# Optimization experiments

Hardware: AMD Instinct MI355X
Metric: run time of the kernel (lower is better)

The kernel has to match this reference:

```python
import jax, jax.numpy as jnp
import numpy as np

N = 4096   # num_nodes == nb_items
E = 3      # num_edge types
C = 2      # num_channels
D = 128    # basket_embed_dim
RU = 128   # rnn_units
B = 32     # batch size
L = 20     # max_seq_length
ALPHA = 0.5


def _gtconv(W, A):
    # softmax over edge types, then channel-weighted combine of adjacencies
    f = jax.nn.softmax(W, axis=1)              # [C, E]
    return jnp.einsum('ce,enm->cnm', f, A)     # [C, N, N]


def _normalize(H):
    # remove self loops, then column-degree (in-degree) inverse normalization
    eye = jnp.eye(H.shape[-1], dtype=H.dtype)
    Hn = H * (1.0 - eye)
    deg = Hn.sum(axis=1)                        # scatter_add over col -> [C, N]
    dinv = jnp.where(deg == 0, jnp.zeros_like(deg), 1.0 / deg)
    dinv = jax.lax.stop_gradient(dinv)          # original computes deg under no_grad
    return Hn * dinv[:, None, :]


def _lstm(x, h0, c0, W_ih, W_hh, b_ih, b_hh):
    # single-layer batch-first LSTM, torch gate order (i, f, g, o)
    def step(carry, xt):
        h, c = carry
        z = xt @ W_ih.T + b_ih + h @ W_hh.T + b_hh
        i, f, g, o = jnp.split(z, 4, axis=-1)
        c = jax.nn.sigmoid(f) * c + jax.nn.sigmoid(i) * jnp.tanh(g)
        h = jax.nn.sigmoid(o) * jnp.tanh(c)
        return (h, c), h
    _, ys = jax.lax.scan(step, (h0, c0), jnp.swapaxes(x, 0, 1))
    return jnp.swapaxes(ys, 0, 1)               # [B, L, RU]


def setup_inputs():
    key = jax.random.key(0)
    k = jax.random.split(key, 12)
    A = jax.random.uniform(k[0], (E, N, N), jnp.float32) * (2.0 / N)
    seqs = (jax.random.uniform(k[1], (B, L, N)) < 0.02).astype(jnp.float32)
    seq_len = jax.random.randint(k[2], (B,), 1, L + 1)
    h0 = jnp.zeros((B, RU), jnp.float32)
    c0 = jnp.zeros((B, RU), jnp.float32)
    W1a = 1.0 + 0.1 * jax.random.normal(k[3], (C, E), jnp.float32)
    W1b = 1.0 + 0.1 * jax.random.normal(k[4], (C, E), jnp.float32)
    W2 = 1.0 + 0.1 * jax.random.normal(k[5], (C, E), jnp.float32)
    I_B = jnp.ones((N,), jnp.float32) / N
    lin_w = jax.random.normal(k[6], (C, D, N), jnp.float32) / np.sqrt(N).astype(np.float32)
    lin_b = jnp.zeros((C, D), jnp.float32)
    proj_w = jax.random.normal(k[7], (D, C * D), jnp.float32) / np.sqrt(C * D).astype(np.float32)
    proj_b = jnp.zeros((D,), jnp.float32)
    W_ih = jax.random.normal(k[8], (4 * RU, D), jnp.float32) / np.sqrt(D).astype(np.float32)
    W_hh = jax.random.normal(k[9], (4 * RU, RU), jnp.float32) / np.sqrt(RU).astype(np.float32)
    b_ih = jnp.zeros((4 * RU,), jnp.float32)
    b_hh = jnp.zeros((4 * RU,), jnp.float32)
    h2item_w = jax.random.normal(k[10], (N, RU), jnp.float32) / np.sqrt(RU).astype(np.float32)
    return dict(A=A, seqs=seqs, seq_len=seq_len, h0=h0, c0=c0, W1a=W1a, W1b=W1b,
                W2=W2, I_B=I_B, lin_w=lin_w, lin_b=lin_b, proj_w=proj_w, proj_b=proj_b,
                W_ih=W_ih, W_hh=W_hh, b_ih=b_ih, b_hh=b_hh, h2item_w=h2item_w)


def reference(A, seqs, seq_len, h0, c0, W1a, W1b, W2, I_B, lin_w, lin_b,
              proj_w, proj_b, W_ih, W_hh, b_ih, b_hh, h2item_w):
    # layer 0 (first=True): H[c] = conv1(A)[c] @ conv2(A)[c]  (spspmm, dense form)
    H = jnp.einsum('cij,cjk->cik', _gtconv(W1a, A), _gtconv(W1b, A))
    # layer 1: H[c] = norm(H)[c] @ conv(A)[c]
    H = jnp.einsum('cij,cjk->cik', _normalize(H), _gtconv(W2, A))

    x = seqs.reshape(-1, N)                     # [B*L, nb_items]
    v = jax.nn.relu(I_B)                        # diag(I_B) after relu
    enc = []
    for i in range(C):
        xh = jax.nn.relu(x @ H[i])
        if i == 0:
            e = jax.nn.relu(x * v) + xh         # note: channel-0 formula differs
        else:
            e = jax.nn.relu(x * v + xh)
        enc.append(e @ lin_w[i].T + lin_b[i])
    enc = jnp.concatenate(enc, axis=1)          # [B*L, C*D]
    baskets = (enc @ proj_w.T + proj_b).reshape(B, L, D)

    lstm_out = _lstm(baskets, h0, c0, W_ih, W_hh, b_ih, b_hh)
    idx = jnp.arange(B) * L + (seq_len - 1)
    last = lstm_out.reshape(-1, RU)[idx]        # [B, RU]
    probs = jax.nn.sigmoid(last @ h2item_w.T)   # [B, nb_items]
    return (1.0 - ALPHA) * probs + ALPHA * (probs * v)
```

## Files before the change

### kernel.cpp

```cpp
#include <hip/hip_runtime.h>


typedef float  f4v  __attribute__((ext_vector_type(4)));
typedef short  s8v  __attribute__((ext_vector_type(8)));
typedef unsigned short u16;
typedef unsigned int u32;
typedef u32    u2v  __attribute__((ext_vector_type(2)));
typedef u32    u4v  __attribute__((ext_vector_type(4)));

#define NN 4096
#define MM 640

__device__ __forceinline__ u16 f2bf(float f){
  unsigned int u = __float_as_uint(f);
  u += 0x7FFFu + ((u>>16)&1u);
  return (u16)(u>>16);
}
__device__ __forceinline__ float bf2f(u16 h){ return __uint_as_float(((unsigned int)h)<<16); }
__device__ __forceinline__ float sigm(float x){ return 1.f/(1.f+__expf(-x)); }

__device__ __forceinline__ u32 pkbf(float lo, float hi){
  u32 r;
  asm("v_cvt_pk_bf16_f32 %0, %1, %2" : "=v"(r) : "v"(lo), "v"(hi));
  return r;
}

__device__ __forceinline__ void gload16(const void* g, void* l){
  __builtin_amdgcn_global_load_lds((const __attribute__((address_space(1))) unsigned int*)g,
                                   (__attribute__((address_space(3))) unsigned int*)l, 16, 0, 0);
}

__device__ __forceinline__ void softmax23(const float* __restrict__ W, float f[2][3]){
  #pragma unroll
  for (int c=0;c<2;c++){
    float a=W[c*3+0], b=W[c*3+1], d=W[c*3+2];
    float m=fmaxf(a,fmaxf(b,d));
    float ea=__expf(a-m), eb=__expf(b-m), ed=__expf(d-m);
    float s=1.f/(ea+eb+ed);
    f[c][0]=ea*s; f[c][1]=eb*s; f[c][2]=ed*s;
  }
}

__global__ __launch_bounds__(256)
void k_combine_all(const float* __restrict__ A, const float* __restrict__ W1a,
                   const float* __restrict__ W1b, const float* __restrict__ W2,
                   u16* __restrict__ C1, u16* __restrict__ C2t,
                   u16* __restrict__ C3t, float* __restrict__ r)
{
  __shared__ u16 t2[64][72];
  __shared__ u16 t3[64][72];
  __shared__ float rs[2][64];
  const int tid = threadIdx.x, lane = tid&63;
  const int n0 = blockIdx.x*64, m0 = blockIdx.y*64;
  float fa[2][3], fb[2][3], fc[2][3];
  softmax23(W1a, fa); softmax23(W1b, fb); softmax23(W2, fc);
  if (tid < 128) rs[tid>>6][tid&63] = 0.f;
  const int mb = tid>>4, nb = tid&15;
  f4v a0[4], a1[4], a2[4];
  #pragma unroll
  for (int j=0;j<4;j++){
    const float* ap = A + (size_t)(m0+mb*4+j)*NN + n0 + nb*4;
    a0[j] = *(const f4v*)ap;
    a1[j] = *(const f4v*)(ap + (size_t)NN*NN);
    a2[j] = *(const f4v*)(ap + 2*(size_t)NN*NN);
  }
  #pragma unroll
  for (int c=0;c<2;c++){
    float rp[4] = {};
    #pragma unroll
    for (int j=0;j<4;j++){
      f4v v1 = fa[c][0]*a0[j] + fa[c][1]*a1[j] + fa[c][2]*a2[j];
      u2v o = { pkbf(v1[0],v1[1]), pkbf(v1[2],v1[3]) };
      *(u2v*)(C1 + ((size_t)c*NN + m0+mb*4+j)*NN + n0 + nb*4) = o;
      #pragma unroll
      for (int k=0;k<4;k++) rp[k] += v1[k];
    }
    #pragma unroll
    for (int jj=0;jj<4;jj++){
      f4v c2v, c3v;
      #pragma unroll
      for (int j=0;j<4;j++){
        c2v[j] = fb[c][0]*a0[j][jj] + fb[c][1]*a1[j][jj] + fb[c][2]*a2[j][jj];
        c3v[j] = fc[c][0]*a0[j][jj] + fc[c][1]*a1[j][jj] + fc[c][2]*a2[j][jj];
      }
      *(u2v*)&t2[nb*4+jj][mb*4] = (u2v){ pkbf(c2v[0],c2v[1]), pkbf(c2v[2],c2v[3]) };
      *(u2v*)&t3[nb*4+jj][mb*4] = (u2v){ pkbf(c3v[0],c3v[1]), pkbf(c3v[2],c3v[3]) };
    }
    __syncthreads();
    #pragma unroll
    for (int rep=0;rep<2;rep++){
      const int rw = rep*32 + (tid>>3), l8 = tid&7;
      *(u4v*)(C2t + ((size_t)c*NN + n0+rw)*NN + m0 + l8*8) = *(const u4v*)&t2[rw][l8*8];
      *(u4v*)(C3t + ((size_t)c*NN + n0+rw)*NN + m0 + l8*8) = *(const u4v*)&t3[rw][l8*8];
    }
    #pragma unroll
    for (int k=0;k<4;k++){
      float v = rp[k];
      v += __shfl_xor(v,16); v += __shfl_xor(v,32);
      if (lane < 16) atomicAdd(&rs[c][nb*4+k], v);
    }
    __syncthreads();
  }
  if (tid < 128) atomicAdd(&r[(size_t)(tid>>6)*NN + n0 + (tid&63)], rs[tid>>6][tid&63]);
}

__global__ __launch_bounds__(256)
void k_sparse_y(const float* __restrict__ seqs, const u16* __restrict__ C1,
                u16* __restrict__ y)
{
  __shared__ int idxl[512];
  __shared__ int scan[256];
  const int tid = threadIdx.x, row = blockIdx.x;
  const float* xr = seqs + (size_t)row*NN;
  int runbase = 0;
  #pragma unroll
  for (int it=0; it<4; ++it){
    f4v v = *(const f4v*)(xr + it*1024 + tid*4);
    int flg[4], loc = 0;
    #pragma unroll
    for (int k=0;k<4;k++){ flg[k] = (v[k] > 0.5f); loc += flg[k]; }
    scan[tid] = loc;
    __syncthreads();
    #pragma unroll
    for (int off=1; off<256; off<<=1){
      int t = (tid>=off) ? scan[tid-off] : 0;
      __syncthreads();
      scan[tid] += t;
      __syncthreads();
    }
    int pos = runbase + scan[tid] - loc;
    #pragma unroll
    for (int k=0;k<4;k++)
      if (flg[k]){ if (pos < 512) idxl[pos] = it*1024 + tid*4 + k; pos++; }
    runbase += scan[255];
    __syncthreads();
  }
  const int nz = runbase < 512 ? runbase : 512;
  float acc0[16], acc1[16];
  #pragma unroll
  for (int k=0;k<16;k++){ acc0[k]=0.f; acc1[k]=0.f; }
  const int cb = tid*16;
  s8v ca, cb8, cc8, cd8;
  if (nz > 0){
    const u16* r0 = C1 + (size_t)idxl[0]*NN + cb;
    const u16* r1 = r0 + (size_t)NN*NN;
    ca=*(const s8v*)r0; cb8=*(const s8v*)(r0+8); cc8=*(const s8v*)r1; cd8=*(const s8v*)(r1+8);
  }
  for (int p=0;p<nz;++p){
    const int pn = (p+1<nz)? p+1 : p;
    const u16* r0 = C1 + (size_t)idxl[pn]*NN + cb;
    const u16* r1 = r0 + (size_t)NN*NN;
    s8v na=*(const s8v*)r0, nb=*(const s8v*)(r0+8), nc=*(const s8v*)r1, nd=*(const s8v*)(r1+8);
    #pragma unroll
    for (int k=0;k<8;k++){
      acc0[k]   += bf2f((u16)ca[k]);
      acc0[8+k] += bf2f((u16)cb8[k]);
      acc1[k]   += bf2f((u16)cc8[k]);
      acc1[8+k] += bf2f((u16)cd8[k]);
    }
    ca=na; cb8=nb; cc8=nc; cd8=nd;
  }
  u4v o0, o1;
  #pragma unroll
  for (int k=0;k<4;k++){
    o0[k] = pkbf(acc0[2*k], acc0[2*k+1]);
    o1[k] = pkbf(acc0[8+2*k], acc0[9+2*k]);
  }
  u16* y0 = y + (size_t)row*NN + cb;
  *(u4v*)y0 = o0; *(u4v*)(y0+8) = o1;
  #pragma unroll
  for (int k=0;k<4;k++){
    o0[k] = pkbf(acc1[2*k], acc1[2*k+1]);
    o1[k] = pkbf(acc1[8+2*k], acc1[9+2*k]);
  }
  u16* y1 = y0 + (size_t)MM*NN;
  *(u4v*)y1 = o0; *(u4v*)(y1+8) = o1;
}

__global__ __launch_bounds__(256)
void k_diagdeg(const u16* __restrict__ C1, const u16* __restrict__ C2t,
               const float* __restrict__ r, float* __restrict__ diag1,
               float* __restrict__ dinv)
{
  const int tid = threadIdx.x, lane = tid&63;
  const int gw = blockIdx.x*4 + (tid>>6);
  const int c = gw>>12, k = gw&4095;
  const u16* p1 = C1  + ((size_t)c*NN + k)*NN;
  const u16* p2 = C2t + ((size_t)c*NN + k)*NN;
  const float* pr = r + (size_t)c*NN;
  float dd = 0.f, dg = 0.f;
  for (int it=0; it<8; ++it){
    const int j = it*512 + lane*8;
    s8v v1 = *(const s8v*)(p1+j);
    s8v v2 = *(const s8v*)(p2+j);
    f4v r0 = *(const f4v*)(pr+j);
    f4v r1 = *(const f4v*)(pr+j+4);
    #pragma unroll
    for (int q=0;q<8;q++){
      float c2 = bf2f((u16)v2[q]);
      dd += bf2f((u16)v1[q]) * c2;
      dg += ((q<4)? r0[q] : r1[q-4]) * c2;
    }
  }
  #pragma unroll
  for (int m=1;m<64;m<<=1){ dd += __shfl_xor(dd, m); dg += __shfl_xor(dg, m); }
  if (lane==0){
    float deg = dg - dd;
    diag1[(size_t)c*NN+k] = dd;
    dinv[(size_t)c*NN+k]  = (deg==0.f) ? 0.f : 1.f/deg;
  }
}

__global__ __launch_bounds__(256)
void k_gemm_sk(const u16* __restrict__ Xb, const u16* __restrict__ Bt,
               float* __restrict__ part)
{
  __shared__ u16 As[2][128*32];
  __shared__ u16 Bs[2][128*32];
  const int tid = threadIdx.x, lane = tid&63, w = tid>>6;
  const int g = blockIdx.x;
  const int xcd = g & 7, q = g >> 3;
  const int m = q % 5, p = q / 5;
  const int nh = p & 3, ks = (p>>2)&3, c = (p>>4)&1;
  const int m0 = m*128, n0 = (nh*8 + xcd)*128, kb = ks*1024;
  const u16* Ab = Xb + (size_t)c*MM*NN;
  const u16* Bb = Bt + (size_t)c*NN*NN;
  const int srow = lane>>2;
  const int scol = ((lane&3) ^ (srow&3))*8;
  const int fr = lane&15, c0 = lane>>4;
  const int wm = (w>>1)*64, wn = (w&1)*64;
  f4v acc[4][4] = {};
  auto STAGE = [&](int buf, int k0){
    #pragma unroll
    for (int i=0;i<2;i++){
      const int rb = i*64 + w*16;
      gload16(Ab + (size_t)(m0 + rb + srow)*NN + k0 + scol, (void*)&As[buf][rb*32]);
      gload16(Bb + (size_t)(n0 + rb + srow)*NN + k0 + scol, (void*)&Bs[buf][rb*32]);
    }
  };
  STAGE(0, kb);
  __syncthreads();
  int cur = 0;
  for (int k0=0;k0<1024;k0+=32){
    if (k0+32 < 1024) STAGE(cur^1, kb+k0+32);
    s8v a[4], b[4];
    #pragma unroll
    for (int t=0;t<4;t++){
      const int ra = wm + t*16 + fr;
      a[t] = *(const s8v*)&As[cur][ra*32 + ((c0 ^ (ra&3))*8)];
      const int rb2 = wn + t*16 + fr;
      b[t] = *(const s8v*)&Bs[cur][rb2*32 + ((c0 ^ (rb2&3))*8)];
    }
    #pragma unroll
    for (int i=0;i<4;i++)
      #pragma unroll
      for (int j=0;j<4;j++)
        acc[i][j] = __builtin_amdgcn_mfma_f32_16x16x32_bf16(a[i], b[j], acc[i][j], 0, 0, 0);
    __syncthreads();
    cur ^= 1;
  }
  float* pb = part + (size_t)(c*4+ks)*MM*NN;
  #pragma unroll
  for (int i=0;i<4;i++){
    #pragma unroll
    for (int j=0;j<4;j++){
      const int col = n0 + wn + j*16 + fr;
      #pragma unroll
      for (int rr=0;rr<4;rr++){
        const int row = m0 + wm + i*16 + (lane>>4)*4 + rr;
        pb[(size_t)row*NN + col] = acc[i][j][rr];
      }
    }
  }
}

template<int M>
__global__ __launch_bounds__(256)
void k_epi(const float* __restrict__ part, const float* __restrict__ seqs,
           const float* __restrict__ diag1, const float* __restrict__ dinv,
           const float* __restrict__ IB, u16* __restrict__ outp)
{
  const int g = blockIdx.x*256 + threadIdx.x;
  const int c = blockIdx.y;
  const int row = g>>10, col = (g&1023)*4;
  const size_t base = (size_t)row*NN + col;
  f4v z = {0.f,0.f,0.f,0.f};
  #pragma unroll
  for (int ks=0;ks<4;ks++)
    z += *(const f4v*)(part + (size_t)(c*4+ks)*MM*NN + base);
  f4v val;
  if constexpr(M==1){
    f4v x  = *(const f4v*)(seqs + base);
    f4v d  = *(const f4v*)(diag1 + (size_t)c*NN + col);
    f4v dv = *(const f4v*)(dinv  + (size_t)c*NN + col);
    val = (z - x*d) * dv;
  } else {
    f4v x  = *(const f4v*)(seqs + base);
    f4v ib = *(const f4v*)(IB + col);
    #pragma unroll
    for (int k=0;k<4;k++){
      float xh = fmaxf(z[k], 0.f);
      float vv = fmaxf(ib[k], 0.f);
      val[k] = (c==0) ? (fmaxf(x[k]*vv,0.f) + xh) : fmaxf(x[k]*vv + xh, 0.f);
    }
  }
  u2v o = { pkbf(val[0],val[1]), pkbf(val[2],val[3]) };
  *(u2v*)(outp + (size_t)c*MM*NN + base) = o;
}

__global__ __launch_bounds__(256)
void k_cvt(const float* __restrict__ linw, const float* __restrict__ whh,
           u16* __restrict__ linwb, u16* __restrict__ whhb)
{
  const int g = blockIdx.x*256 + threadIdx.x;
  const int i = g*4;
  const int NL = 2*128*NN;
  f4v v; u16* dst;
  if (i < NL){ v = *(const f4v*)(linw + i); dst = linwb + i; }
  else       { v = *(const f4v*)(whh + (i-NL)); dst = whhb + (i-NL); }
  u2v o = { pkbf(v[0],v[1]), pkbf(v[2],v[3]) };
  *(u2v*)dst = o;
}

__global__ __launch_bounds__(256)
void k_lin(const u16* __restrict__ e, const u16* __restrict__ linwb,
           float* __restrict__ encr)
{
  __shared__ u16 As[64*32];
  __shared__ u16 Bs[64*32];
  const int tid=threadIdx.x, lane=tid&63, w=tid>>6;
  const int m0 = blockIdx.x*64, d0 = blockIdx.y*64;
  const int c = blockIdx.z>>4, ks = blockIdx.z&15;
  const u16* Ab = e + (size_t)c*MM*NN;
  const u16* Bb = linwb + (size_t)c*128*NN;
  const int srow=lane>>2, skof=(lane&3)*8, fr=lane&15, fk=(lane>>4)*8;
  const int wm=(w>>1)*32, wn=(w&1)*32;
  f4v acc[2][2];
  #pragma unroll
  for (int i=0;i<2;i++)
    #pragma unroll
    for (int j=0;j<2;j++) acc[i][j] = (f4v){0.f,0.f,0.f,0.f};
  for (int ki=0;ki<8;++ki){
    const int k0 = ks*256 + ki*32;
    gload16(Ab + (size_t)(m0 + w*16 + srow)*NN + k0 + skof, (void*)&As[(w*16)*32]);
    gload16(Bb + (size_t)(d0 + w*16 + srow)*NN + k0 + skof, (void*)&Bs[(w*16)*32]);
    __syncthreads();
    s8v a[2], b[2];
    #pragma unroll
    for (int t=0;t<2;t++) a[t] = *(const s8v*)&As[(wm+t*16+fr)*32+fk];
    #pragma unroll
    for (int t=0;t<2;t++) b[t] = *(const s8v*)&Bs[(wn+t*16+fr)*32+fk];
    #pragma unroll
    for (int i=0;i<2;i++)
      #pragma unroll
      for (int j=0;j<2;j++)
        acc[i][j] = __builtin_amdgcn_mfma_f32_16x16x32_bf16(a[i], b[j], acc[i][j], 0, 0, 0);
    __syncthreads();
  }
  #pragma unroll
  for (int i=0;i<2;i++)
    #pragma unroll
    for (int j=0;j<2;j++){
      const int col = d0 + wn + j*16 + fr;
      #pragma unroll
      for (int rr=0;rr<4;rr++){
        const int row = m0 + wm + i*16 + (lane>>4)*4 + rr;
        atomicAdd(&encr[(size_t)row*256 + c*128 + col], acc[i][j][rr]);
      }
    }
}

__global__ __launch_bounds__(256)
void k_proj(const float* __restrict__ encr, const float* __restrict__ linb,
            const float* __restrict__ pw, const float* __restrict__ pb,
            float* __restrict__ bask)
{
  const int g = blockIdx.x*256 + threadIdx.x;
  const int row = g>>7, d = g&127;
  const float* er = encr + (size_t)row*256;
  const float* wr = pw + (size_t)d*256;
  float acc = pb[d];
  for (int j=0;j<256;j+=4){
    f4v e4 = *(const f4v*)(er+j);
    f4v l4 = *(const f4v*)(linb+j);
    f4v w4 = *(const f4v*)(wr+j);
    acc += (e4[0]+l4[0])*w4[0] + (e4[1]+l4[1])*w4[1] + (e4[2]+l4[2])*w4[2] + (e4[3]+l4[3])*w4[3];
  }
  bask[g] = acc;
}

__global__ __launch_bounds__(256)
void k_xhat(const float* __restrict__ bask, const float* __restrict__ wih,
            const float* __restrict__ bih, const float* __restrict__ bhh,
            float* __restrict__ xh)
{
  const int g = blockIdx.x*256 + threadIdx.x;
  const int row = g>>9, n = g&511;
  const float* br = bask + (size_t)row*128;
  const float* wr = wih + (size_t)n*128;
  float acc = bih[n] + bhh[n];
  for (int k=0;k<128;k+=4){
    f4v b4=*(const f4v*)(br+k); f4v w4=*(const f4v*)(wr+k);
    acc += b4[0]*w4[0]+b4[1]*w4[1]+b4[2]*w4[2]+b4[3]*w4[3];
  }
  const int b = row/20, t = row%20;
  xh[((size_t)t*32 + b)*512 + n] = acc;
}

__global__ __launch_bounds__(512)
void k_lstm(const float* __restrict__ xhat, const u16* __restrict__ whhb,
            const float* __restrict__ h0, const float* __restrict__ c0,
            const int* __restrict__ slen, float* __restrict__ last)
{
  __shared__ float zb[32][512];
  __shared__ float cbuf[32][128];
  __shared__ u16 hb[32][136];
  const int tid = threadIdx.x, lane = tid&63, w = tid>>6;
  for (int i=tid; i<4096; i+=512){ int b=i>>7,u=i&127; cbuf[b][u]=c0[i]; hb[b][u]=f2bf(h0[i]); }
  const int fr = lane&15, fko = (lane>>4)*8;
  s8v bfr[4][4];
  #pragma unroll
  for (int nt=0;nt<4;nt++)
    #pragma unroll
    for (int kf=0;kf<4;kf++)
      bfr[nt][kf] = *(const s8v*)(whhb + (size_t)(w*64 + nt*16 + fr)*128 + kf*32 + fko);
  __syncthreads();
  for (int t=0;t<20;++t){
    s8v af[2][4];
    #pragma unroll
    for (int mt=0;mt<2;mt++)
      #pragma unroll
      for (int kf=0;kf<4;kf++)
        af[mt][kf] = *(const s8v*)&hb[mt*16+fr][kf*32+fko];
    f4v z[2][4];
    #pragma unroll
    for (int mt=0;mt<2;mt++)
      #pragma unroll
      for (int nt=0;nt<4;nt++){
        const int nn2 = w*64 + nt*16 + fr;
        #pragma unroll
        for (int rr=0;rr<4;rr++){
          const int bb = mt*16 + (lane>>4)*4 + rr;
          z[mt][nt][rr] = xhat[((size_t)t*32 + bb)*512 + nn2];
        }
      }
    #pragma unroll
    for (int kf=0;kf<4;kf++)
      #pragma unroll
      for (int mt=0;mt<2;mt++)
        #pragma unroll
        for (int nt=0;nt<4;nt++)
          z[mt][nt] = __builtin_amdgcn_mfma_f32_16x16x32_bf16(af[mt][kf], bfr[nt][kf], z[mt][nt], 0, 0, 0);
    #pragma unroll
    for (int mt=0;mt<2;mt++)
      #pragma unroll
      for (int nt=0;nt<4;nt++){
        const int nn2 = w*64 + nt*16 + fr;
        #pragma unroll
        for (int rr=0;rr<4;rr++){
          const int bb = mt*16 + (lane>>4)*4 + rr;
          zb[bb][nn2] = z[mt][nt][rr];
        }
      }
    __syncthreads();
    for (int p=tid; p<4096; p+=512){
      const int b=p>>7, u=p&127;
      float zi=zb[b][u], zf=zb[b][128+u], zg=zb[b][256+u], zo=zb[b][384+u];
      float ii=sigm(zi), ff=sigm(zf), gg=tanhf(zg), oo=sigm(zo);
      float cn = ff*cbuf[b][u] + ii*gg;
      float hn = oo*tanhf(cn);
      cbuf[b][u]=cn; hb[b][u]=f2bf(hn);
      if (t == slen[b]-1) last[p] = hn;
    }
    __syncthreads();
  }
}

__global__ __launch_bounds__(256)
void k_final(const float* __restrict__ last, const float* __restrict__ h2w,
             const float* __restrict__ IB, float* __restrict__ out)
{
  __shared__ float ls[128];
  const int b = blockIdx.y;
  const int n = blockIdx.x*256 + threadIdx.x;
  if (threadIdx.x < 128) ls[threadIdx.x] = last[b*128 + threadIdx.x];
  __syncthreads();
  const float* wr = h2w + (size_t)n*128;
  float acc = 0.f;
  for (int k=0;k<128;k+=4){
    f4v w4 = *(const f4v*)(wr+k);
    acc += w4[0]*ls[k] + w4[1]*ls[k+1] + w4[2]*ls[k+2] + w4[3]*ls[k+3];
  }
  const float vn = fmaxf(IB[n], 0.f);
  out[(size_t)b*NN + n] = (0.5f + 0.5f*vn) * sigm(acc);
}

extern "C" void kernel_launch(void* const* d_in, const int* in_sizes, int n_in,
                              void* d_out, int out_size, void* d_ws, size_t ws_size,
                              hipStream_t stream)
{
  const float* A    = (const float*)d_in[0];
  const float* seqs = (const float*)d_in[1];
  const int*   slen = (const int*)  d_in[2];
  const float* h0   = (const float*)d_in[3];
  const float* c0   = (const float*)d_in[4];
  const float* W1a  = (const float*)d_in[5];
  const float* W1b  = (const float*)d_in[6];
  const float* W2   = (const float*)d_in[7];
  const float* IB   = (const float*)d_in[8];
  const float* linw = (const float*)d_in[9];
  const float* linb = (const float*)d_in[10];
  const float* pw   = (const float*)d_in[11];
  const float* pb   = (const float*)d_in[12];
  const float* wih  = (const float*)d_in[13];
  const float* whh  = (const float*)d_in[14];
  const float* bih  = (const float*)d_in[15];
  const float* bhh  = (const float*)d_in[16];
  const float* h2w  = (const float*)d_in[17];
  (void)in_sizes; (void)n_in; (void)out_size; (void)ws_size;

  char* ws = (char*)d_ws;
  size_t off = 0;
  auto alloc = [&](size_t sz)->void*{ void* p = ws + off; off += (sz + 255) & ~(size_t)255; return p; };
  u16*   C1    = (u16*)  alloc((size_t)2*NN*NN*2);
  u16*   C2t   = (u16*)  alloc((size_t)2*NN*NN*2);
  u16*   C3t   = (u16*)  alloc((size_t)2*NN*NN*2);
  u16*   y     = (u16*)  alloc((size_t)2*MM*NN*2);
  u16*   u     = (u16*)  alloc((size_t)2*MM*NN*2);
  float* part  = (float*)alloc((size_t)4*2*MM*NN*4);
  float* r     = (float*)alloc((size_t)2*NN*4);
  float* diag1 = (float*)alloc((size_t)2*NN*4);
  float* dinv  = (float*)alloc((size_t)2*NN*4);
  u16*   linwb = (u16*)  alloc((size_t)2*128*NN*2);
  u16*   whhb  = (u16*)  alloc((size_t)512*128*2);
  float* encr  = (float*)alloc((size_t)MM*256*4);
  float* bask  = (float*)alloc((size_t)MM*128*4);
  float* xh    = (float*)alloc((size_t)20*32*512*4);
  float* last  = (float*)alloc((size_t)32*128*4);

  hipMemsetAsync(r, 0, (size_t)2*NN*4, stream);
  hipMemsetAsync(encr, 0, (size_t)MM*256*4, stream);

  k_combine_all<<<dim3(64,64),256,0,stream>>>(A, W1a, W1b, W2, C1, C2t, C3t, r);
  k_sparse_y<<<MM,256,0,stream>>>(seqs, C1, y);
  k_diagdeg<<<2048,256,0,stream>>>(C1, C2t, r, diag1, dinv);
  k_gemm_sk<<<1280,256,0,stream>>>(y, C2t, part);
  k_epi<1><<<dim3(2560,2),256,0,stream>>>(part, seqs, diag1, dinv, IB, u);
  k_gemm_sk<<<1280,256,0,stream>>>(u, C3t, part);
  u16* e = y;
  k_epi<2><<<dim3(2560,2),256,0,stream>>>(part, seqs, diag1, dinv, IB, e);
  k_cvt<<<1088,256,0,stream>>>(linw, whh, linwb, whhb);
  k_lin<<<dim3(10,2,32),256,0,stream>>>(e, linwb, encr);
  k_proj<<<320,256,0,stream>>>(encr, linb, pw, pb, bask);
  k_xhat<<<1280,256,0,stream>>>(bask, wih, bih, bhh, xh);
  k_lstm<<<1,512,0,stream>>>(xh, whhb, h0, c0, slen, last);
  k_final<<<dim3(16,32),256,0,stream>>>(last, h2w, IB, (float*)d_out);
}
```

Baseline: 531.2 us.

## Split combine kernel and co-schedule independent stages in shared launches

The single combine kernel is split so only the C1 combination and row sums run first. The C2t/C3t transpose-combine, the sparse y accumulation and the weight bf16 conversion now run as disjoint block ranges of one launch. The diag/degree reduction runs as extra blocks inside the first split-K GEMM. This cuts launch count and lets independent work fill the GPU concurrently, at the cost of re-reading A in a second pass and heterogeneous blocks competing for resources.

```diff
diff --git a/kernel.cpp b/kernel.cpp
--- a/kernel.cpp
+++ b/kernel.cpp
@@ -42,18 +42,14 @@
 }
 
 __global__ __launch_bounds__(256)
-void k_combine_all(const float* __restrict__ A, const float* __restrict__ W1a,
-                   const float* __restrict__ W1b, const float* __restrict__ W2,
-                   u16* __restrict__ C1, u16* __restrict__ C2t,
-                   u16* __restrict__ C3t, float* __restrict__ r)
-{
-  __shared__ u16 t2[64][72];
-  __shared__ u16 t3[64][72];
+void k_comb1(const float* __restrict__ A, const float* __restrict__ W1a,
+             u16* __restrict__ C1, float* __restrict__ r)
+{
   __shared__ float rs[2][64];
   const int tid = threadIdx.x, lane = tid&63;
   const int n0 = blockIdx.x*64, m0 = blockIdx.y*64;
-  float fa[2][3], fb[2][3], fc[2][3];
-  softmax23(W1a, fa); softmax23(W1b, fb); softmax23(W2, fc);
+  float fa[2][3];
+  softmax23(W1a, fa);
   if (tid < 128) rs[tid>>6][tid&63] = 0.f;
   const int mb = tid>>4, nb = tid&15;
   f4v a0[4], a1[4], a2[4];
@@ -64,160 +60,200 @@
     a1[j] = *(const f4v*)(ap + (size_t)NN*NN);
     a2[j] = *(const f4v*)(ap + 2*(size_t)NN*NN);
   }
+  float rp[2][4] = {};
   #pragma unroll
   for (int c=0;c<2;c++){
-    float rp[4] = {};
     #pragma unroll
     for (int j=0;j<4;j++){
       f4v v1 = fa[c][0]*a0[j] + fa[c][1]*a1[j] + fa[c][2]*a2[j];
       u2v o = { pkbf(v1[0],v1[1]), pkbf(v1[2],v1[3]) };
       *(u2v*)(C1 + ((size_t)c*NN + m0+mb*4+j)*NN + n0 + nb*4) = o;
       #pragma unroll
-      for (int k=0;k<4;k++) rp[k] += v1[k];
-    }
-    #pragma unroll
-    for (int jj=0;jj<4;jj++){
-      f4v c2v, c3v;
-      #pragma unroll
-      for (int j=0;j<4;j++){
-        c2v[j] = fb[c][0]*a0[j][jj] + fb[c][1]*a1[j][jj] + fb[c][2]*a2[j][jj];
-        c3v[j] = fc[c][0]*a0[j][jj] + fc[c][1]*a1[j][jj] + fc[c][2]*a2[j][jj];
-      }
-      *(u2v*)&t2[nb*4+jj][mb*4] = (u2v){ pkbf(c2v[0],c2v[1]), pkbf(c2v[2],c2v[3]) };
-      *(u2v*)&t3[nb*4+jj][mb*4] = (u2v){ pkbf(c3v[0],c3v[1]), pkbf(c3v[2],c3v[3]) };
-    }
-    __syncthreads();
-    #pragma unroll
-    for (int rep=0;rep<2;rep++){
-      const int rw = rep*32 + (tid>>3), l8 = tid&7;
-      *(u4v*)(C2t + ((size_t)c*NN + n0+rw)*NN + m0 + l8*8) = *(const u4v*)&t2[rw][l8*8];
-      *(u4v*)(C3t + ((size_t)c*NN + n0+rw)*NN + m0 + l8*8) = *(const u4v*)&t3[rw][l8*8];
-    }
+      for (int k=0;k<4;k++) rp[c][k] += v1[k];
+    }
+  }
+  __syncthreads();
+  #pragma unroll
+  for (int c=0;c<2;c++)
     #pragma unroll
     for (int k=0;k<4;k++){
-      float v = rp[k];
+      float v = rp[c][k];
       v += __shfl_xor(v,16); v += __shfl_xor(v,32);
       if (lane < 16) atomicAdd(&rs[c][nb*4+k], v);
     }
-    __syncthreads();
-  }
+  __syncthreads();
   if (tid < 128) atomicAdd(&r[(size_t)(tid>>6)*NN + n0 + (tid&63)], rs[tid>>6][tid&63]);
 }
 
 __global__ __launch_bounds__(256)
-void k_sparse_y(const float* __restrict__ seqs, const u16* __restrict__ C1,
-                u16* __restrict__ y)
+void k_m2(const float* __restrict__ A, const float* __restrict__ W1b,
+          const float* __restrict__ W2, const float* __restrict__ seqs,
+          const u16* __restrict__ C1, const float* __restrict__ linw,
+          const float* __restrict__ whh, u16* __restrict__ C2t,
+          u16* __restrict__ C3t, u16* __restrict__ y,
+          u16* __restrict__ linwb, u16* __restrict__ whhb)
 {
   __shared__ int idxl[512];
   __shared__ int scan[256];
-  const int tid = threadIdx.x, row = blockIdx.x;
-  const float* xr = seqs + (size_t)row*NN;
-  int runbase = 0;
-  #pragma unroll
-  for (int it=0; it<4; ++it){
-    f4v v = *(const f4v*)(xr + it*1024 + tid*4);
-    int flg[4], loc = 0;
-    #pragma unroll
-    for (int k=0;k<4;k++){ flg[k] = (v[k] > 0.5f); loc += flg[k]; }
-    scan[tid] = loc;
-    __syncthreads();
-    #pragma unroll
-    for (int off=1; off<256; off<<=1){
-      int t = (tid>=off) ? scan[tid-off] : 0;
+  __shared__ u16 t2[64][72];
+  __shared__ u16 t3[64][72];
+  const int g = blockIdx.x, tid = threadIdx.x;
+  if (g < MM){
+    const int row = g;
+    const float* xr = seqs + (size_t)row*NN;
+    int runbase = 0;
+    #pragma unroll
+    for (int it=0; it<4; ++it){
+      f4v v = *(const f4v*)(xr + it*1024 + tid*4);
+      int flg[4], loc = 0;
+      #pragma unroll
+      for (int k=0;k<4;k++){ flg[k] = (v[k] > 0.5f); loc += flg[k]; }
+      scan[tid] = loc;
       __syncthreads();
-      scan[tid] += t;
+      #pragma unroll
+      for (int off=1; off<256; off<<=1){
+        int t = (tid>=off) ? scan[tid-off] : 0;
+        __syncthreads();
+        scan[tid] += t;
+        __syncthreads();
+      }
+      int pos = runbase + scan[tid] - loc;
+      #pragma unroll
+      for (int k=0;k<4;k++)
+        if (flg[k]){ if (pos < 512) idxl[pos] = it*1024 + tid*4 + k; pos++; }
+      runbase += scan[255];
       __syncthreads();
     }
-    int pos = runbase + scan[tid] - loc;
-    #pragma unroll
-    for (int k=0;k<4;k++)
-      if (flg[k]){ if (pos < 512) idxl[pos] = it*1024 + tid*4 + k; pos++; }
-    runbase += scan[255];
-    __syncthreads();
-  }
-  const int nz = runbase < 512 ? runbase : 512;
-  float acc0[16], acc1[16];
-  #pragma unroll
-  for (int k=0;k<16;k++){ acc0[k]=0.f; acc1[k]=0.f; }
-  const int cb = tid*16;
-  s8v ca, cb8, cc8, cd8;
-  if (nz > 0){
-    const u16* r0 = C1 + (size_t)idxl[0]*NN + cb;
-    const u16* r1 = r0 + (size_t)NN*NN;
-    ca=*(const s8v*)r0; cb8=*(const s8v*)(r0+8); cc8=*(const s8v*)r1; cd8=*(const s8v*)(r1+8);
-  }
-  for (int p=0;p<nz;++p){
-    const int pn = (p+1<nz)? p+1 : p;
-    const u16* r0 = C1 + (size_t)idxl[pn]*NN + cb;
-    const u16* r1 = r0 + (size_t)NN*NN;
-    s8v na=*(const s8v*)r0, nb=*(const s8v*)(r0+8), nc=*(const s8v*)r1, nd=*(const s8v*)(r1+8);
-    #pragma unroll
-    for (int k=0;k<8;k++){
-      acc0[k]   += bf2f((u16)ca[k]);
-      acc0[8+k] += bf2f((u16)cb8[k]);
-      acc1[k]   += bf2f((u16)cc8[k]);
-      acc1[8+k] += bf2f((u16)cd8[k]);
-    }
-    ca=na; cb8=nb; cc8=nc; cd8=nd;
-  }
-  u4v o0, o1;
-  #pragma unroll
-  for (int k=0;k<4;k++){
-    o0[k] = pkbf(acc0[2*k], acc0[2*k+1]);
-    o1[k] = pkbf(acc0[8+2*k], acc0[9+2*k]);
-  }
-  u16* y0 = y + (size_t)row*NN + cb;
-  *(u4v*)y0 = o0; *(u4v*)(y0+8) = o1;
-  #pragma unroll
-  for (int k=0;k<4;k++){
-    o0[k] = pkbf(acc1[2*k], acc1[2*k+1]);
-    o1[k] = pkbf(acc1[8+2*k], acc1[9+2*k]);
-  }
-  u16* y1 = y0 + (size_t)MM*NN;
-  *(u4v*)y1 = o0; *(u4v*)(y1+8) = o1;
-}
-
-__global__ __launch_bounds__(256)
-void k_diagdeg(const u16* __restrict__ C1, const u16* __restrict__ C2t,
+    const int nz = runbase < 512 ? runbase : 512;
+    float acc0[16], acc1[16];
+    #pragma unroll
+    for (int k=0;k<16;k++){ acc0[k]=0.f; acc1[k]=0.f; }
+    const int cb = tid*16;
+    s8v ca, cb8, cc8, cd8;
+    if (nz > 0){
+      const u16* r0 = C1 + (size_t)idxl[0]*NN + cb;
+      const u16* r1 = r0 + (size_t)NN*NN;
+      ca=*(const s8v*)r0; cb8=*(const s8v*)(r0+8); cc8=*(const s8v*)r1; cd8=*(const s8v*)(r1+8);
+    }
+    for (int p=0;p<nz;++p){
+      const int pn = (p+1<nz)? p+1 : p;
+      const u16* r0 = C1 + (size_t)idxl[pn]*NN + cb;
+      const u16* r1 = r0 + (size_t)NN*NN;
+      s8v na=*(const s8v*)r0, nb=*(const s8v*)(r0+8), nc=*(const s8v*)r1, nd=*(const s8v*)(r1+8);
+      #pragma unroll
+      for (int k=0;k<8;k++){
+        acc0[k]   += bf2f((u16)ca[k]);
+        acc0[8+k] += bf2f((u16)cb8[k]);
+        acc1[k]   += bf2f((u16)cc8[k]);
+        acc1[8+k] += bf2f((u16)cd8[k]);
+      }
+      ca=na; cb8=nb; cc8=nc; cd8=nd;
+    }
+    u4v o0, o1;
+    #pragma unroll
+    for (int k=0;k<4;k++){
+      o0[k] = pkbf(acc0[2*k], acc0[2*k+1]);
+      o1[k] = pkbf(acc0[8+2*k], acc0[9+2*k]);
+    }
+    u16* y0 = y + (size_t)row*NN + cb;
+    *(u4v*)y0 = o0; *(u4v*)(y0+8) = o1;
+    #pragma unroll
+    for (int k=0;k<4;k++){
+      o0[k] = pkbf(acc1[2*k], acc1[2*k+1]);
+      o1[k] = pkbf(acc1[8+2*k], acc1[9+2*k]);
+    }
+    u16* y1 = y0 + (size_t)MM*NN;
+    *(u4v*)y1 = o0; *(u4v*)(y1+8) = o1;
+  } else if (g < MM + 4096){
+    const int t = g - MM;
+    const int n0 = (t & 63)*64, m0 = (t >> 6)*64;
+    const int lane = tid&63;
+    float fb[2][3], fc[2][3];
+    softmax23(W1b, fb); softmax23(W2, fc);
+    const int mb = tid>>4, nb = tid&15;
+    f4v a0[4], a1[4], a2[4];
+    #pragma unroll
+    for (int j=0;j<4;j++){
+      const float* ap = A + (size_t)(m0+mb*4+j)*NN + n0 + nb*4;
+      a0[j] = *(const f4v*)ap;
+      a1[j] = *(const f4v*)(ap + (size_t)NN*NN);
+      a2[j] = *(const f4v*)(ap + 2*(size_t)NN*NN);
+    }
+    (void)lane;
+    #pragma unroll
+    for (int c=0;c<2;c++){
+      #pragma unroll
+      for (int jj=0;jj<4;jj++){
+        f4v c2v, c3v;
+        #pragma unroll
+        for (int j=0;j<4;j++){
+          c2v[j] = fb[c][0]*a0[j][jj] + fb[c][1]*a1[j][jj] + fb[c][2]*a2[j][jj];
+          c3v[j] = fc[c][0]*a0[j][jj] + fc[c][1]*a1[j][jj] + fc[c][2]*a2[j][jj];
+        }
+        *(u2v*)&t2[nb*4+jj][mb*4] = (u2v){ pkbf(c2v[0],c2v[1]), pkbf(c2v[2],c2v[3]) };
+        *(u2v*)&t3[nb*4+jj][mb*4] = (u2v){ pkbf(c3v[0],c3v[1]), pkbf(c3v[2],c3v[3]) };
+      }
+      __syncthreads();
+      #pragma unroll
+      for (int rep=0;rep<2;rep++){
+        const int rw = rep*32 + (tid>>3), l8 = tid&7;
+        *(u4v*)(C2t + ((size_t)c*NN + n0+rw)*NN + m0 + l8*8) = *(const u4v*)&t2[rw][l8*8];
+        *(u4v*)(C3t + ((size_t)c*NN + n0+rw)*NN + m0 + l8*8) = *(const u4v*)&t3[rw][l8*8];
+      }
+      __syncthreads();
+    }
+  } else {
+    const int b = g - (MM + 4096);
+    const int i = (b*256 + tid)*4;
+    const int NL = 2*128*NN;
+    f4v v; u16* dst;
+    if (i < NL){ v = *(const f4v*)(linw + i); dst = linwb + i; }
+    else       { v = *(const f4v*)(whh + (i-NL)); dst = whhb + (i-NL); }
+    u2v o = { pkbf(v[0],v[1]), pkbf(v[2],v[3]) };
+    *(u2v*)dst = o;
+  }
+}
+
+template<int WITHDIAG>
+__global__ __launch_bounds__(256)
+void k_gemm_sk(const u16* __restrict__ Xb, const u16* __restrict__ Bt,
+               float* __restrict__ part, const u16* __restrict__ C1,
                const float* __restrict__ r, float* __restrict__ diag1,
                float* __restrict__ dinv)
 {
   const int tid = threadIdx.x, lane = tid&63;
-  const int gw = blockIdx.x*4 + (tid>>6);
-  const int c = gw>>12, k = gw&4095;
-  const u16* p1 = C1  + ((size_t)c*NN + k)*NN;
-  const u16* p2 = C2t + ((size_t)c*NN + k)*NN;
-  const float* pr = r + (size_t)c*NN;
-  float dd = 0.f, dg = 0.f;
-  for (int it=0; it<8; ++it){
-    const int j = it*512 + lane*8;
-    s8v v1 = *(const s8v*)(p1+j);
-    s8v v2 = *(const s8v*)(p2+j);
-    f4v r0 = *(const f4v*)(pr+j);
-    f4v r1 = *(const f4v*)(pr+j+4);
-    #pragma unroll
-    for (int q=0;q<8;q++){
-      float c2 = bf2f((u16)v2[q]);
-      dd += bf2f((u16)v1[q]) * c2;
-      dg += ((q<4)? r0[q] : r1[q-4]) * c2;
-    }
-  }
-  #pragma unroll
-  for (int m=1;m<64;m<<=1){ dd += __shfl_xor(dd, m); dg += __shfl_xor(dg, m); }
-  if (lane==0){
-    float deg = dg - dd;
-    diag1[(size_t)c*NN+k] = dd;
-    dinv[(size_t)c*NN+k]  = (deg==0.f) ? 0.f : 1.f/deg;
-  }
-}
-
-__global__ __launch_bounds__(256)
-void k_gemm_sk(const u16* __restrict__ Xb, const u16* __restrict__ Bt,
-               float* __restrict__ part)
-{
+  if (WITHDIAG && blockIdx.x >= 1280){
+    const int gw = (blockIdx.x-1280)*4 + (tid>>6);
+    const int c = gw>>12, k = gw&4095;
+    const u16* p1 = C1 + ((size_t)c*NN + k)*NN;
+    const u16* p2 = Bt + ((size_t)c*NN + k)*NN;
+    const float* pr = r + (size_t)c*NN;
+    float dd = 0.f, dg = 0.f;
+    for (int it=0; it<8; ++it){
+      const int j = it*512 + lane*8;
+      s8v v1 = *(const s8v*)(p1+j);
+      s8v v2 = *(const s8v*)(p2+j);
+      f4v r0 = *(const f4v*)(pr+j);
+      f4v r1 = *(const f4v*)(pr+j+4);
+      #pragma unroll
+      for (int q=0;q<8;q++){
+        float c2 = bf2f((u16)v2[q]);
+        dd += bf2f((u16)v1[q]) * c2;
+        dg += ((q<4)? r0[q] : r1[q-4]) * c2;
+      }
+    }
+    #pragma unroll
+    for (int m=1;m<64;m<<=1){ dd += __shfl_xor(dd, m); dg += __shfl_xor(dg, m); }
+    if (lane==0){
+      float deg = dg - dd;
+      diag1[(size_t)c*NN+k] = dd;
+      dinv[(size_t)c*NN+k]  = (deg==0.f) ? 0.f : 1.f/deg;
+    }
+    return;
+  }
   __shared__ u16 As[2][128*32];
   __shared__ u16 Bs[2][128*32];
-  const int tid = threadIdx.x, lane = tid&63, w = tid>>6;
+  const int w = tid>>6;
   const int g = blockIdx.x;
   const int xcd = g & 7, q = g >> 3;
   const int m = q % 5, p = q / 5;
@@ -306,20 +342,6 @@
   }
   u2v o = { pkbf(val[0],val[1]), pkbf(val[2],val[3]) };
   *(u2v*)(outp + (size_t)c*MM*NN + base) = o;
-}
-
-__global__ __launch_bounds__(256)
-void k_cvt(const float* __restrict__ linw, const float* __restrict__ whh,
-           u16* __restrict__ linwb, u16* __restrict__ whhb)
-{
-  const int g = blockIdx.x*256 + threadIdx.x;
-  const int i = g*4;
-  const int NL = 2*128*NN;
-  f4v v; u16* dst;
-  if (i < NL){ v = *(const f4v*)(linw + i); dst = linwb + i; }
-  else       { v = *(const f4v*)(whh + (i-NL)); dst = whhb + (i-NL); }
-  u2v o = { pkbf(v[0],v[1]), pkbf(v[2],v[3]) };
-  *(u2v*)dst = o;
 }
 
 __global__ __launch_bounds__(256)
@@ -541,15 +563,14 @@
   hipMemsetAsync(r, 0, (size_t)2*NN*4, stream);
   hipMemsetAsync(encr, 0, (size_t)MM*256*4, stream);
 
-  k_combine_all<<<dim3(64,64),256,0,stream>>>(A, W1a, W1b, W2, C1, C2t, C3t, r);
-  k_sparse_y<<<MM,256,0,stream>>>(seqs, C1, y);
-  k_diagdeg<<<2048,256,0,stream>>>(C1, C2t, r, diag1, dinv);
-  k_gemm_sk<<<1280,256,0,stream>>>(y, C2t, part);
+  k_comb1<<<dim3(64,64),256,0,stream>>>(A, W1a, C1, r);
+  k_m2<<<MM + 4096 + 1088,256,0,stream>>>(A, W1b, W2, seqs, C1, linw, whh,
+                                          C2t, C3t, y, linwb, whhb);
+  k_gemm_sk<1><<<1280+2048,256,0,stream>>>(y, C2t, part, C1, r, diag1, dinv);
   k_epi<1><<<dim3(2560,2),256,0,stream>>>(part, seqs, diag1, dinv, IB, u);
-  k_gemm_sk<<<1280,256,0,stream>>>(u, C3t, part);
+  k_gemm_sk<0><<<1280,256,0,stream>>>(u, C3t, part, C1, r, diag1, dinv);
   u16* e = y;
   k_epi<2><<<dim3(2560,2),256,0,stream>>>(part, seqs, diag1, dinv, IB, e);
-  k_cvt<<<1088,256,0,stream>>>(linw, whh, linwb, whhb);
   k_lin<<<dim3(10,2,32),256,0,stream>>>(e, linwb, encr);
   k_proj<<<320,256,0,stream>>>(encr, linb, pw, pb, bask);
   k_xhat<<<1280,256,0,stream>>>(bask, wih, bih, bhh, xh);
```

Result: slower. 567.4 us (+6.8%).

## Fuse split-K reduction epilogue into GEMM via last-block atomic counter

Applied to the files above, without the earlier changes.

Removes the two separate epilogue kernels. Each split-K GEMM block now fences its writes and bumps an atomic counter for its output tile. The fourth block to finish sums the partials and applies the normalization or activation epilogue, writing the bf16 result. This saves two launches and lets the reduction start while other tiles are still running, at the cost of extra fences and atomics and a serialized tail on the last block per tile.

```diff
diff --git a/kernel.cpp b/kernel.cpp
--- a/kernel.cpp
+++ b/kernel.cpp
@@ -211,12 +211,17 @@
   }
 }
 
+template<int M>
 __global__ __launch_bounds__(256)
 void k_gemm_sk(const u16* __restrict__ Xb, const u16* __restrict__ Bt,
-               float* __restrict__ part)
+               float* __restrict__ part, const float* __restrict__ seqs,
+               const float* __restrict__ diag1, const float* __restrict__ dinv,
+               const float* __restrict__ IB, u16* __restrict__ outp,
+               int* __restrict__ cnt)
 {
   __shared__ u16 As[2][128*32];
   __shared__ u16 Bs[2][128*32];
+  __shared__ int done;
   const int tid = threadIdx.x, lane = tid&63, w = tid>>6;
   const int g = blockIdx.x;
   const int xcd = g & 7, q = g >> 3;
@@ -272,40 +277,39 @@
       }
     }
   }
-}
-
-template<int M>
-__global__ __launch_bounds__(256)
-void k_epi(const float* __restrict__ part, const float* __restrict__ seqs,
-           const float* __restrict__ diag1, const float* __restrict__ dinv,
-           const float* __restrict__ IB, u16* __restrict__ outp)
-{
-  const int g = blockIdx.x*256 + threadIdx.x;
-  const int c = blockIdx.y;
-  const int row = g>>10, col = (g&1023)*4;
-  const size_t base = (size_t)row*NN + col;
-  f4v z = {0.f,0.f,0.f,0.f};
-  #pragma unroll
-  for (int ks=0;ks<4;ks++)
-    z += *(const f4v*)(part + (size_t)(c*4+ks)*MM*NN + base);
-  f4v val;
-  if constexpr(M==1){
-    f4v x  = *(const f4v*)(seqs + base);
-    f4v d  = *(const f4v*)(diag1 + (size_t)c*NN + col);
-    f4v dv = *(const f4v*)(dinv  + (size_t)c*NN + col);
-    val = (z - x*d) * dv;
-  } else {
-    f4v x  = *(const f4v*)(seqs + base);
-    f4v ib = *(const f4v*)(IB + col);
-    #pragma unroll
-    for (int k=0;k<4;k++){
-      float xh = fmaxf(z[k], 0.f);
-      float vv = fmaxf(ib[k], 0.f);
-      val[k] = (c==0) ? (fmaxf(x[k]*vv,0.f) + xh) : fmaxf(x[k]*vv + xh, 0.f);
-    }
-  }
-  u2v o = { pkbf(val[0],val[1]), pkbf(val[2],val[3]) };
-  *(u2v*)(outp + (size_t)c*MM*NN + base) = o;
+  __threadfence();
+  __syncthreads();
+  if (tid == 0) done = atomicAdd(&cnt[(c*5 + m)*32 + nh*8 + xcd], 1);
+  __syncthreads();
+  if (done != 3) return;
+  __threadfence();
+  for (int idx = tid; idx < 128*32; idx += 256){
+    const int row = m0 + (idx>>5);
+    const int col = n0 + (idx&31)*4;
+    const size_t base = (size_t)row*NN + col;
+    f4v z = {0.f,0.f,0.f,0.f};
+    #pragma unroll
+    for (int k2=0;k2<4;k2++)
+      z += *(const f4v*)(part + (size_t)(c*4+k2)*MM*NN + base);
+    f4v val;
+    if constexpr(M==1){
+      f4v x  = *(const f4v*)(seqs + base);
+      f4v d  = *(const f4v*)(diag1 + (size_t)c*NN + col);
+      f4v dv = *(const f4v*)(dinv  + (size_t)c*NN + col);
+      val = (z - x*d) * dv;
+    } else {
+      f4v x  = *(const f4v*)(seqs + base);
+      f4v ib = *(const f4v*)(IB + col);
+      #pragma unroll
+      for (int k2=0;k2<4;k2++){
+        float xh = fmaxf(z[k2], 0.f);
+        float vv = fmaxf(ib[k2], 0.f);
+        val[k2] = (c==0) ? (fmaxf(x[k2]*vv,0.f) + xh) : fmaxf(x[k2]*vv + xh, 0.f);
+      }
+    }
+    u2v o = { pkbf(val[0],val[1]), pkbf(val[2],val[3]) };
+    *(u2v*)(outp + (size_t)c*MM*NN + base) = o;
+  }
 }
 
 __global__ __launch_bounds__(256)
@@ -531,6 +535,7 @@
   float* r     = (float*)alloc((size_t)2*NN*4);
   float* diag1 = (float*)alloc((size_t)2*NN*4);
   float* dinv  = (float*)alloc((size_t)2*NN*4);
+  int*   cnt   = (int*)  alloc((size_t)2*320*4);
   u16*   linwb = (u16*)  alloc((size_t)2*128*NN*2);
   u16*   whhb  = (u16*)  alloc((size_t)512*128*2);
   float* encr  = (float*)alloc((size_t)MM*256*4);
@@ -539,16 +544,15 @@
   float* last  = (float*)alloc((size_t)32*128*4);
 
   hipMemsetAsync(r, 0, (size_t)2*NN*4, stream);
+  hipMemsetAsync(cnt, 0, (size_t)2*320*4, stream);
   hipMemsetAsync(encr, 0, (size_t)MM*256*4, stream);
 
   k_combine_all<<<dim3(64,64),256,0,stream>>>(A, W1a, W1b, W2, C1, C2t, C3t, r);
   k_sparse_y<<<MM,256,0,stream>>>(seqs, C1, y);
   k_diagdeg<<<2048,256,0,stream>>>(C1, C2t, r, diag1, dinv);
-  k_gemm_sk<<<1280,256,0,stream>>>(y, C2t, part);
-  k_epi<1><<<dim3(2560,2),256,0,stream>>>(part, seqs, diag1, dinv, IB, u);
-  k_gemm_sk<<<1280,256,0,stream>>>(u, C3t, part);
+  k_gemm_sk<1><<<1280,256,0,stream>>>(y, C2t, part, seqs, diag1, dinv, IB, u, cnt);
+  k_gemm_sk<2><<<1280,256,0,stream>>>(u, C3t, part, seqs, diag1, dinv, IB, y, cnt + 320);
   u16* e = y;
-  k_epi<2><<<dim3(2560,2),256,0,stream>>>(part, seqs, diag1, dinv, IB, e);
   k_cvt<<<1088,256,0,stream>>>(linw, whh, linwb, whhb);
   k_lin<<<dim3(10,2,32),256,0,stream>>>(e, linwb, encr);
   k_proj<<<320,256,0,stream>>>(encr, linb, pw, pb, bask);
```

Result: slower. 1.024 ms (+92.7%).
